# Performance work log

Measured on AMD Instinct MI355X. Metric: run time of the kernel, lower is better.

The kernel has to match this reference:

```python
import jax, jax.numpy as jnp
import numpy as np

D = 1024
B, S = 4, 4096


def setup_inputs() -> dict:
    key = jax.random.key(0)
    ks = jax.random.split(key, 5)
    scale = 1.0 / np.sqrt(D)  # ~ torch Linear init magnitude
    return {
        "x": jax.random.normal(ks[0], (B, S, D), dtype=jnp.float32),
        "Wa": jax.random.normal(ks[1], (D, D), dtype=jnp.float32) * scale,
        "Wb": jax.random.normal(ks[2], (D, D), dtype=jnp.float32) * scale,
        "Wc": jax.random.normal(ks[3], (D, D), dtype=jnp.float32) * scale,
        "Wd": jax.random.normal(ks[4], (D, D), dtype=jnp.float32) * scale,
    }


def reference(x, Wa, Wb, Wc, Wd):
    # torch nn.Linear(bias=False): y = x @ W.T, W is [out, in]
    A = jax.nn.relu(jnp.einsum("bsd,ed->bse", x, Wa))
    Bm = jax.nn.relu(jnp.einsum("bsd,ed->bse", x, Wb))
    C = jax.nn.relu(jnp.einsum("bsd,ed->bse", x, Wc))
    cmp_matrix = jnp.einsum("bse,bte->bst", A, Bm)  # [B,S,S] unnormalized scores
    out = jnp.einsum("bst,bte->bse", cmp_matrix, C)
    return jax.nn.relu(jnp.einsum("bsd,ed->bse", out, Wd))
```

## Files before the change

### kernel.cpp

```cpp
#include <hip/hip_runtime.h>
#include <hip/hip_bf16.h>

#define D_ 1024
#define B_ 4
#define S_ 4096

typedef __attribute__((ext_vector_type(8))) short bf16x8;
typedef __attribute__((ext_vector_type(4))) float f32x4;
typedef __attribute__((ext_vector_type(4))) unsigned int u32x4;
typedef __attribute__((ext_vector_type(4))) unsigned short u16x4;

__device__ __forceinline__ unsigned short f2bf(float f) {
    unsigned int u = __builtin_bit_cast(unsigned int, f);
    u = u + 0x7fffu + ((u >> 16) & 1u);
    return (unsigned short)(u >> 16);
}
__device__ __forceinline__ unsigned int pk2(float a, float b) {
    return (unsigned int)f2bf(a) | ((unsigned int)f2bf(b) << 16);
}
__device__ __forceinline__ float bf2f(unsigned short h) {
    unsigned int u = ((unsigned int)h) << 16;
    return __builtin_bit_cast(float, u);
}
__device__ __forceinline__ void gload16(const void* g, void* l) {
    __builtin_amdgcn_global_load_lds(
        (const __attribute__((address_space(1))) void*)g,
        (__attribute__((address_space(3))) void*)l, 16, 0, 0);
}

__device__ __forceinline__ void conv8(const float* s, unsigned short* d, size_t j) {
    f32x4 v0 = *(const f32x4*)(s + j);
    f32x4 v1 = *(const f32x4*)(s + j + 4);
    u32x4 o;
    o[0] = pk2(v0[0], v0[1]);
    o[1] = pk2(v0[2], v0[3]);
    o[2] = pk2(v1[0], v1[1]);
    o[3] = pk2(v1[2], v1[3]);
    *(u32x4*)(d + j) = o;
}

__global__ __launch_bounds__(256)
void conv_all(const float* __restrict__ x, const float* __restrict__ Wb,
              const float* __restrict__ Wc,
              unsigned short* __restrict__ xb, unsigned short* __restrict__ wbb,
              unsigned short* __restrict__ wcb, int n8x, int n8w) {
    int i = blockIdx.x * blockDim.x + threadIdx.x;
    const int stride = gridDim.x * blockDim.x;
    const int ntot = n8x + 2 * n8w;
    for (; i < ntot; i += stride) {
        if (i < n8x)                conv8(x,  xb,  (size_t)i * 8);
        else if (i < n8x + n8w)     conv8(Wb, wbb, (size_t)(i - n8x) * 8);
        else                        conv8(Wc, wcb, (size_t)(i - n8x - n8w) * 8);
    }
}

__global__ __launch_bounds__(256)
void reduce_convw(const unsigned short* __restrict__ P, unsigned short* __restrict__ E,
                  const float* __restrict__ Wd, const float* __restrict__ Wa,
                  unsigned short* __restrict__ wdb, unsigned short* __restrict__ wab,
                  int n8e, int n8w) {
    int t = blockIdx.x * blockDim.x + threadIdx.x;
    const int stride = gridDim.x * blockDim.x;
    const int DD = D_ * D_;
    const int ntot = n8e + 2 * n8w;
    for (; t < ntot; t += stride) {
        if (t < n8e) {
            size_t idx = (size_t)t * 8;
            int b = (int)(idx / DD);
            size_t i = idx % DD;
            float s[8];
#pragma unroll
            for (int k = 0; k < 8; ++k) s[k] = 0.f;
#pragma unroll
            for (int seg = 0; seg < 4; ++seg) {
                const unsigned short* p = P + (size_t)(b * 4 + seg) * DD + i;
                u16x4 v0 = *(const u16x4*)p;
                u16x4 v1 = *(const u16x4*)(p + 4);
#pragma unroll
                for (int k = 0; k < 4; ++k) { s[k] += bf2f(v0[k]); s[4 + k] += bf2f(v1[k]); }
            }
            u16x4 o0, o1;
#pragma unroll
            for (int k = 0; k < 4; ++k) { o0[k] = f2bf(s[k]); o1[k] = f2bf(s[4 + k]); }
            *(u16x4*)(E + idx) = o0;
            *(u16x4*)(E + idx + 4) = o1;
        } else if (t < n8e + n8w) {
            conv8(Wd, wdb, (size_t)(t - n8e) * 8);
        } else {
            conv8(Wa, wab, (size_t)(t - n8e - n8w) * 8);
        }
    }
}

#define BM 128
#define BN 128
#define BK 64
#define NTHR 256

template<bool OUT_F32, bool TRANS, bool RELU>
__global__ __launch_bounds__(NTHR)
void gemm_nt(const unsigned short* __restrict__ Ap, const unsigned short* __restrict__ Bp,
             void* __restrict__ Op, int M, int N, int K, int klen, int split,
             long long sA, long long sB, long long sO)
{
    __shared__ char lds_a[BM * BK * 2];
    __shared__ char lds_b[BN * BK * 2];

    const int tid   = threadIdx.x;
    const int bz    = blockIdx.z;
    const int batch = bz / split;
    const int k0    = (bz % split) * klen;
    const int bm    = blockIdx.y * BM;
    const int bn    = blockIdx.x * BN;

    const unsigned short* Abase = Ap + (size_t)batch * sA + (size_t)bm * K;
    const unsigned short* Bbase = Bp + (size_t)batch * sB + (size_t)bn * K;

    const int lane = tid & 63;
    const int wave = tid >> 6;
    const int wm   = (wave >> 1) * 64;
    const int wn   = (wave & 1) * 64;
    const int l16  = lane & 15;
    const int lhi  = lane >> 4;

    const int schnk = (lane & 7) ^ (lane >> 3);
    const char* gA0 = (const char*)(Abase + (size_t)(wave * 32 + (lane >> 3)) * K) + schnk * 16;
    const char* gB0 = (const char*)(Bbase + (size_t)(wave * 32 + (lane >> 3)) * K) + schnk * 16;
    char* lA0 = lds_a + wave * 4096;
    char* lB0 = lds_b + wave * 4096;

    f32x4 acc[4][4];
#pragma unroll
    for (int i = 0; i < 4; ++i)
#pragma unroll
        for (int j = 0; j < 4; ++j)
            acc[i][j] = (f32x4){0.f, 0.f, 0.f, 0.f};

    for (int kt = k0; kt < k0 + klen; kt += BK) {
#pragma unroll
        for (int p = 0; p < 4; ++p)
            gload16(gA0 + ((size_t)p * 8 * K + kt) * 2, lA0 + p * 1024);
#pragma unroll
        for (int p = 0; p < 4; ++p)
            gload16(gB0 + ((size_t)p * 8 * K + kt) * 2, lB0 + p * 1024);
        __syncthreads();
#pragma unroll
        for (int kk = 0; kk < BK / 32; ++kk) {
            bf16x8 af[4], bfr[4];
#pragma unroll
            for (int i = 0; i < 4; ++i) {
                int row = wm + i * 16 + l16;
                int byt = (row * 128 + kk * 64 + lhi * 16) ^ ((row & 7) << 4);
                af[i] = *(const bf16x8*)(lds_a + byt);
            }
#pragma unroll
            for (int j = 0; j < 4; ++j) {
                int row = wn + j * 16 + l16;
                int byt = (row * 128 + kk * 64 + lhi * 16) ^ ((row & 7) << 4);
                bfr[j] = *(const bf16x8*)(lds_b + byt);
            }
#pragma unroll
            for (int i = 0; i < 4; ++i)
#pragma unroll
                for (int j = 0; j < 4; ++j)
                    acc[i][j] = __builtin_amdgcn_mfma_f32_16x16x32_bf16(af[i], bfr[j], acc[i][j], 0, 0, 0);
        }
        __syncthreads();
    }

    const size_t obase = (size_t)bz * (size_t)sO;
    if constexpr (!TRANS) {
#pragma unroll
        for (int i = 0; i < 4; ++i) {
            const int m0 = bm + wm + i * 16 + lhi * 4;
#pragma unroll
            for (int j = 0; j < 4; ++j) {
                const int n = bn + wn + j * 16 + l16;
#pragma unroll
                for (int r = 0; r < 4; ++r) {
                    float v = acc[i][j][r];
                    if constexpr (RELU) v = fmaxf(v, 0.f);
                    size_t addr = obase + (size_t)(m0 + r) * N + n;
                    if constexpr (OUT_F32) ((float*)Op)[addr] = v;
                    else ((unsigned short*)Op)[addr] = f2bf(v);
                }
            }
        }
    } else {
#pragma unroll
        for (int i = 0; i < 4; ++i) {
            const int m0 = bm + wm + i * 16 + lhi * 4;
#pragma unroll
            for (int j = 0; j < 4; ++j) {
                const int n = bn + wn + j * 16 + l16;
                u16x4 h;
#pragma unroll
                for (int r = 0; r < 4; ++r) {
                    float v = acc[i][j][r];
                    if constexpr (RELU) v = fmaxf(v, 0.f);
                    h[r] = f2bf(v);
                }
                *(u16x4*)((unsigned short*)Op + obase + (size_t)n * M + m0) = h;
            }
        }
    }
}

#define CTILE 65536
#define CBOFF 32768

template<bool OUT_F32, bool TRANS, bool RELU>
__global__ __launch_bounds__(512, 2)
void gemm256(const unsigned short* __restrict__ Ap, const unsigned short* __restrict__ Bp,
             void* __restrict__ Op, int M, int N, int K, int klen, int split,
             long long sA, long long sB, long long sO)
{
    __shared__ char lds[131072];
    const int tid  = threadIdx.x;
    const int wave = tid >> 6;
    const int lane = tid & 63;

    const int gx = gridDim.x, gy = gridDim.y;
    const int f   = blockIdx.x + gx * (blockIdx.y + gy * blockIdx.z);
    const int nwg = gx * gy * (int)gridDim.z;
    const int s   = (f & 7) * (nwg >> 3) + (f >> 3);
    const int lx  = s % gx;
    const int lyz = s / gx;
    const int ly  = lyz % gy;
    const int lz  = lyz / gy;

    const int batch = lz / split;
    const int k0    = (lz % split) * klen;
    const int bm    = ly * 256;
    const int bn    = lx * 256;

    const int wm  = (wave >> 2) * 128;
    const int wn  = (wave & 3) * 64;
    const int l16 = lane & 15, lhi = lane >> 4;

    const unsigned short* Abase = Ap + (size_t)batch * sA + (size_t)bm * K;
    const unsigned short* Bbase = Bp + (size_t)batch * sB + (size_t)bn * K;
    const int srow  = lane >> 3;
    const int schnk = (lane & 7) ^ srow;
    const size_t K2 = (size_t)K * 2;
    const char* gA = (const char*)Abase + (size_t)srow * K2 + (size_t)schnk * 16 + (size_t)k0 * 2;
    const char* gB = (const char*)Bbase + (size_t)srow * K2 + (size_t)schnk * 16 + (size_t)k0 * 2;

    const int lxor = (l16 & 7) << 4;
    const int aX = (wm + l16) * 128 + lhi * 16;
    const int bX = (wn + l16) * 128 + lhi * 16;
    const char* aB00 = lds + 0 * CTILE + ((aX + 0 * 64) ^ lxor);
    const char* aB01 = lds + 0 * CTILE + ((aX + 1 * 64) ^ lxor);
    const char* aB10 = lds + 1 * CTILE + ((aX + 0 * 64) ^ lxor);
    const char* aB11 = lds + 1 * CTILE + ((aX + 1 * 64) ^ lxor);
    const char* bB00 = lds + 0 * CTILE + CBOFF + ((bX + 0 * 64) ^ lxor);
    const char* bB01 = lds + 0 * CTILE + CBOFF + ((bX + 1 * 64) ^ lxor);
    const char* bB10 = lds + 1 * CTILE + CBOFF + ((bX + 0 * 64) ^ lxor);
    const char* bB11 = lds + 1 * CTILE + CBOFF + ((bX + 1 * 64) ^ lxor);

    f32x4 acc[8][4];
#pragma unroll
    for (int i = 0; i < 8; ++i)
#pragma unroll
        for (int j = 0; j < 4; ++j)
            acc[i][j] = (f32x4){0.f, 0.f, 0.f, 0.f};

    bf16x8 a[4][2], b0[2][2], b1[2][2];

    auto stageA2 = [&](int c, int t, int h) {
#pragma unroll
        for (int p = 0; p < 2; ++p)
            gload16(gA + (size_t)t * 128 + (size_t)(h * 128 + wave * 16 + p * 8) * K2,
                    lds + c * CTILE + h * 16384 + wave * 2048 + p * 1024);
    };
    auto stageB2 = [&](int c, int t, int h) {
#pragma unroll
        for (int p = 0; p < 2; ++p)
            gload16(gB + (size_t)t * 128 + (size_t)(h * 128 + wave * 16 + p * 8) * K2,
                    lds + c * CTILE + CBOFF + h * 16384 + wave * 2048 + p * 1024);
    };
    auto ldAh = [&](int c, int mh, int lo) {
        const char* base0 = c ? aB10 : aB00;
        const char* base1 = c ? aB11 : aB01;
#pragma unroll
        for (int i4 = 0; i4 < 2; ++i4) {
            const int imm = (mh * 64 + (lo + i4) * 16) * 128;
            a[lo + i4][0] = *(const bf16x8*)(base0 + imm);
            a[lo + i4][1] = *(const bf16x8*)(base1 + imm);
        }
    };
    auto ldBh = [&](int c, int nh, bf16x8 (&bb)[2][2], int j2) {
        const char* base0 = c ? bB10 : bB00;
        const char* base1 = c ? bB11 : bB01;
        const int imm = (nh * 32 + j2 * 16) * 128;
        bb[j2][0] = *(const bf16x8*)(base0 + imm);
        bb[j2][1] = *(const bf16x8*)(base1 + imm);
    };
    auto ldB = [&](int c, int nh, bf16x8 (&bb)[2][2]) {
        ldBh(c, nh, bb, 0); ldBh(c, nh, bb, 1);
    };
    auto mmH = [&](int mh, int nh, bf16x8 (&bb)[2][2], int lo) {
        __builtin_amdgcn_s_setprio(1);
#pragma unroll
        for (int i4 = 0; i4 < 2; ++i4)
#pragma unroll
            for (int j2 = 0; j2 < 2; ++j2)
#pragma unroll
                for (int kk = 0; kk < 2; ++kk)
                    acc[mh * 4 + lo + i4][nh * 2 + j2] = __builtin_amdgcn_mfma_f32_16x16x32_bf16(
                        a[lo + i4][kk], bb[j2][kk], acc[mh * 4 + lo + i4][nh * 2 + j2], 0, 0, 0);
        __builtin_amdgcn_s_setprio(0);
    };
    auto mm = [&](int mh, int nh, bf16x8 (&bb)[2][2]) { mmH(mh, nh, bb, 0); mmH(mh, nh, bb, 2); };

#define BAR()   __builtin_amdgcn_s_barrier()
#define LGKM0() asm volatile("s_waitcnt lgkmcnt(0)" ::: "memory")
#define VM2()   asm volatile("s_waitcnt vmcnt(2)" ::: "memory")
#define VM4()   asm volatile("s_waitcnt vmcnt(4)" ::: "memory")
#define VM6()   asm volatile("s_waitcnt vmcnt(6)" ::: "memory")

    const int NT = klen / 64;
    stageB2(0, 0, 0); stageB2(0, 0, 1); stageA2(0, 0, 0); stageA2(0, 0, 1);
    stageB2(1, 1, 0); stageB2(1, 1, 1); stageA2(1, 1, 0);
    VM6();
    BAR();
    ldB(0, 0, b0); ldAh(0, 0, 0); ldAh(0, 0, 2);

    for (int itr = 0; itr < NT / 2; ++itr) {
        const int t1  = 2 * itr + 1;
        const int tp0 = (2 * itr + 2) % NT;
        const int tp1 = (2 * itr + 3) % NT;
        LGKM0(); mmH(0, 0, b0, 0);
        ldBh(0, 1, b1, 0);
        mmH(0, 0, b0, 2);
        ldBh(0, 1, b1, 1); stageA2(1, t1, 1);
        BAR();
        LGKM0(); mmH(0, 1, b1, 0);
        ldAh(0, 1, 0);
        mmH(0, 1, b1, 2);
        ldAh(0, 1, 2); VM4();
        BAR();
        LGKM0(); mm(1, 0, b0);
        ldB(1, 0, b0); stageB2(0, tp0, 0); VM2();
        BAR();
        LGKM0(); mmH(1, 1, b1, 0);
        ldAh(1, 0, 0);
        mmH(1, 1, b1, 2);
        ldAh(1, 0, 2); stageB2(0, tp0, 1); stageA2(0, tp0, 0);
        BAR();
        LGKM0(); mmH(0, 0, b0, 0);
        ldBh(1, 1, b1, 0);
        mmH(0, 0, b0, 2);
        ldBh(1, 1, b1, 1); stageA2(0, tp0, 1);
        BAR();
        LGKM0(); mmH(0, 1, b1, 0);
        ldAh(1, 1, 0);
        mmH(0, 1, b1, 2);
        ldAh(1, 1, 2); VM4();
        BAR();
        LGKM0(); mm(1, 0, b0);
        ldB(0, 0, b0); stageB2(1, tp1, 0); VM2();
        BAR();
        LGKM0(); mmH(1, 1, b1, 0);
        ldAh(0, 0, 0);
        mmH(1, 1, b1, 2);
        ldAh(0, 0, 2); stageB2(1, tp1, 1); stageA2(1, tp1, 0);
        BAR();
    }
    asm volatile("s_waitcnt vmcnt(0)" ::: "memory");

    const size_t obase = (size_t)lz * (size_t)sO;
    if constexpr (!TRANS) {
#pragma unroll
        for (int i = 0; i < 8; ++i) {
            const int m0 = bm + wm + i * 16 + lhi * 4;
#pragma unroll
            for (int j = 0; j < 4; ++j) {
                const int n = bn + wn + j * 16 + l16;
#pragma unroll
                for (int r = 0; r < 4; ++r) {
                    float v = acc[i][j][r];
                    if constexpr (RELU) v = fmaxf(v, 0.f);
                    size_t addr = obase + (size_t)(m0 + r) * N + n;
                    if constexpr (OUT_F32) ((float*)Op)[addr] = v;
                    else ((unsigned short*)Op)[addr] = f2bf(v);
                }
            }
        }
    } else {
#pragma unroll
        for (int i = 0; i < 8; ++i) {
            const int m0 = bm + wm + i * 16 + lhi * 4;
#pragma unroll
            for (int j = 0; j < 4; ++j) {
                const int n = bn + wn + j * 16 + l16;
                u16x4 h;
#pragma unroll
                for (int r = 0; r < 4; ++r) {
                    float v = acc[i][j][r];
                    if constexpr (RELU) v = fmaxf(v, 0.f);
                    h[r] = f2bf(v);
                }
                *(u16x4*)((unsigned short*)Op + obase + (size_t)n * M + m0) = h;
            }
        }
    }
#undef BAR
#undef LGKM0
#undef VM2
#undef VM4
#undef VM6
}

extern "C" void kernel_launch(void* const* d_in, const int* in_sizes, int n_in,
                              void* d_out, int out_size, void* d_ws, size_t ws_size,
                              hipStream_t stream) {
    (void)in_sizes; (void)n_in; (void)out_size; (void)ws_size;
    const float* x  = (const float*)d_in[0];
    const float* Wa = (const float*)d_in[1];
    const float* Wb = (const float*)d_in[2];
    const float* Wc = (const float*)d_in[3];
    const float* Wd = (const float*)d_in[4];

    const long long SD  = (long long)S_ * D_;
    const long long DD2 = (long long)D_ * D_;
    const size_t MB = 1024 * 1024;

    unsigned short* BC    = (unsigned short*)d_ws;
    unsigned short* Enorm = (unsigned short*)d_ws;
    unsigned short* Ao    = (unsigned short*)d_ws;
    unsigned short* Ft    = (unsigned short*)((char*)d_ws + 32 * MB);
    unsigned short* Wdb   = (unsigned short*)((char*)d_ws + 40 * MB);
    unsigned short* Wab   = (unsigned short*)((char*)d_ws + 42 * MB);
    char* ob = (char*)d_out;
    unsigned short* xb  = (unsigned short*)ob;
    unsigned short* Pp  = (unsigned short*)(ob + 32 * MB);
    unsigned short* Wbb = (unsigned short*)(ob + 56 * MB);
    unsigned short* Wcb = (unsigned short*)(ob + 58 * MB);

    dim3 blk256(256, 1, 1);
    dim3 blk512(512, 1, 1);
    dim3 gBC(2048 / 256, S_ / 256, B_);
    dim3 gE(D_ / 256, D_ / 256, B_ * 4);
    dim3 gS(D_ / 256, S_ / 256, B_);
    dim3 gF(D_ / BN, D_ / BM, B_);

    const int n8x = (B_ * S_ * D_) / 8;
    const int n8w = (D_ * D_) / 8;
    const int n8e = (B_ * D_ * D_) / 8;

    conv_all<<<2048, blk256, 0, stream>>>(x, Wb, Wc, xb, Wbb, Wcb, n8x, n8w);
    gemm256<false, true,  true ><<<gBC, blk512, 0, stream>>>(xb, Wbb, BC, S_, 2048, D_, D_, 1, SD, 0, 2 * SD);
    gemm256<false, false, false><<<gE, blk512, 0, stream>>>(BC, BC + SD, Pp, D_, D_, S_, S_ / 4, 4, 2 * SD, 2 * SD, DD2);
    reduce_convw<<<1024, blk256, 0, stream>>>(Pp, Enorm, Wd, Wa, Wdb, Wab, n8e, n8w);
    gemm_nt<false, true,  false><<<gF, blk256, 0, stream>>>(Enorm, Wdb, Ft, D_, D_, D_, D_, 1, DD2, 0, DD2);
    gemm256<false, false, true ><<<gS, blk512, 0, stream>>>(xb, Wab, Ao, S_, D_, D_, D_, 1, SD, 0, SD);
    gemm256<true,  false, true ><<<gS, blk512, 0, stream>>>(Ao, Ft, (float*)d_out, S_, D_, D_, D_, 1, SD, DD2, SD);
}
```

Measured before the change: 237.7 us.

## Add 16-wave 256x256 GEMM variant and use it for the BC and E stages

Introduces a 1024-thread (16-wave) version of the 256x256-tile bf16 MFMA GEMM, where each wave computes a 64x64 sub-tile, with a reworked double-buffered LDS staging and barrier schedule. The two large GEMMs (B/C projection and the split-K A^T-style product) now launch this kernel instead of the 512-thread version. The aim is more waves in flight to hide LDS and global latency and to spread MFMA work. The cost is more barriers per k-step, a smaller per-wave tile with less register reuse, and tighter register limits from 1024-thread launch bounds.

```diff
diff --git a/kernel.cpp b/kernel.cpp
--- a/kernel.cpp
+++ b/kernel.cpp
@@ -412,6 +412,200 @@
 #undef VM6
 }
 
+template<bool OUT_F32, bool TRANS, bool RELU>
+__global__ __launch_bounds__(1024, 4)
+void gemm256w16(const unsigned short* __restrict__ Ap, const unsigned short* __restrict__ Bp,
+                void* __restrict__ Op, int M, int N, int K, int klen, int split,
+                long long sA, long long sB, long long sO)
+{
+    __shared__ char lds[131072];
+    const int tid  = threadIdx.x;
+    const int wave = tid >> 6;
+    const int lane = tid & 63;
+
+    const int gx = gridDim.x, gy = gridDim.y;
+    const int f   = blockIdx.x + gx * (blockIdx.y + gy * blockIdx.z);
+    const int nwg = gx * gy * (int)gridDim.z;
+    const int s   = (f & 7) * (nwg >> 3) + (f >> 3);
+    const int lx  = s % gx;
+    const int lyz = s / gx;
+    const int ly  = lyz % gy;
+    const int lz  = lyz / gy;
+
+    const int batch = lz / split;
+    const int k0    = (lz % split) * klen;
+    const int bm    = ly * 256;
+    const int bn    = lx * 256;
+
+    const int wm  = (wave >> 2) * 64;
+    const int wn  = (wave & 3) * 64;
+    const int l16 = lane & 15, lhi = lane >> 4;
+
+    const unsigned short* Abase = Ap + (size_t)batch * sA + (size_t)bm * K;
+    const unsigned short* Bbase = Bp + (size_t)batch * sB + (size_t)bn * K;
+    const int srowB = tid >> 3;
+    const int schnk = (lane & 7) ^ (lane >> 3);
+    const size_t K2 = (size_t)K * 2;
+    const char* gA = (const char*)Abase + (size_t)srowB * K2 + (size_t)schnk * 16 + (size_t)k0 * 2;
+    const char* gB = (const char*)Bbase + (size_t)srowB * K2 + (size_t)schnk * 16 + (size_t)k0 * 2;
+
+    const int lxor = (l16 & 7) << 4;
+    const int aX = (wm + l16) * 128 + lhi * 16;
+    const int bX = (wn + l16) * 128 + lhi * 16;
+    const char* aB00 = lds + 0 * CTILE + ((aX + 0 * 64) ^ lxor);
+    const char* aB01 = lds + 0 * CTILE + ((aX + 1 * 64) ^ lxor);
+    const char* aB10 = lds + 1 * CTILE + ((aX + 0 * 64) ^ lxor);
+    const char* aB11 = lds + 1 * CTILE + ((aX + 1 * 64) ^ lxor);
+    const char* bB00 = lds + 0 * CTILE + CBOFF + ((bX + 0 * 64) ^ lxor);
+    const char* bB01 = lds + 0 * CTILE + CBOFF + ((bX + 1 * 64) ^ lxor);
+    const char* bB10 = lds + 1 * CTILE + CBOFF + ((bX + 0 * 64) ^ lxor);
+    const char* bB11 = lds + 1 * CTILE + CBOFF + ((bX + 1 * 64) ^ lxor);
+
+    f32x4 acc[4][4];
+#pragma unroll
+    for (int i = 0; i < 4; ++i)
+#pragma unroll
+        for (int j = 0; j < 4; ++j)
+            acc[i][j] = (f32x4){0.f, 0.f, 0.f, 0.f};
+
+    bf16x8 a[2][2], b0[2][2], b1[2][2];
+
+    auto stageA2 = [&](int c, int t, int h) {
+        gload16(gA + (size_t)t * 128 + (size_t)(h * 128) * K2,
+                lds + c * CTILE + h * 16384 + wave * 1024);
+    };
+    auto stageB2 = [&](int c, int t, int h) {
+        gload16(gB + (size_t)t * 128 + (size_t)(h * 128) * K2,
+                lds + c * CTILE + CBOFF + h * 16384 + wave * 1024);
+    };
+    auto ldAh = [&](int c, int mh, int q) {
+        const char* base0 = c ? aB10 : aB00;
+        const char* base1 = c ? aB11 : aB01;
+        const int imm = (mh * 32 + q * 16) * 128;
+        a[q][0] = *(const bf16x8*)(base0 + imm);
+        a[q][1] = *(const bf16x8*)(base1 + imm);
+    };
+    auto ldBh = [&](int c, int nh, bf16x8 (&bb)[2][2], int j2) {
+        const char* base0 = c ? bB10 : bB00;
+        const char* base1 = c ? bB11 : bB01;
+        const int imm = (nh * 32 + j2 * 16) * 128;
+        bb[j2][0] = *(const bf16x8*)(base0 + imm);
+        bb[j2][1] = *(const bf16x8*)(base1 + imm);
+    };
+    auto ldB = [&](int c, int nh, bf16x8 (&bb)[2][2]) {
+        ldBh(c, nh, bb, 0); ldBh(c, nh, bb, 1);
+    };
+    auto mmH = [&](int mh, int nh, bf16x8 (&bb)[2][2], int q) {
+        __builtin_amdgcn_s_setprio(1);
+#pragma unroll
+        for (int j2 = 0; j2 < 2; ++j2)
+#pragma unroll
+            for (int kk = 0; kk < 2; ++kk)
+                acc[mh * 2 + q][nh * 2 + j2] = __builtin_amdgcn_mfma_f32_16x16x32_bf16(
+                    a[q][kk], bb[j2][kk], acc[mh * 2 + q][nh * 2 + j2], 0, 0, 0);
+        __builtin_amdgcn_s_setprio(0);
+    };
+    auto mm = [&](int mh, int nh, bf16x8 (&bb)[2][2]) { mmH(mh, nh, bb, 0); mmH(mh, nh, bb, 1); };
+
+#define BAR()   __builtin_amdgcn_s_barrier()
+#define LGKM0() asm volatile("s_waitcnt lgkmcnt(0)" ::: "memory")
+#define VM1()   asm volatile("s_waitcnt vmcnt(1)" ::: "memory")
+#define VM2()   asm volatile("s_waitcnt vmcnt(2)" ::: "memory")
+#define VM3()   asm volatile("s_waitcnt vmcnt(3)" ::: "memory")
+
+    const int NT = klen / 64;
+    stageB2(0, 0, 0); stageB2(0, 0, 1); stageA2(0, 0, 0); stageA2(0, 0, 1);
+    stageB2(1, 1, 0); stageB2(1, 1, 1); stageA2(1, 1, 0);
+    VM3();
+    BAR();
+    ldB(0, 0, b0); ldAh(0, 0, 0); ldAh(0, 0, 1);
+
+    for (int itr = 0; itr < NT / 2; ++itr) {
+        const int t1  = 2 * itr + 1;
+        const int tp0 = (2 * itr + 2) % NT;
+        const int tp1 = (2 * itr + 3) % NT;
+        LGKM0(); mmH(0, 0, b0, 0);
+        ldBh(0, 1, b1, 0);
+        mmH(0, 0, b0, 1);
+        ldBh(0, 1, b1, 1); stageA2(1, t1, 1);
+        BAR();
+        LGKM0(); mmH(0, 1, b1, 0);
+        ldAh(0, 1, 0);
+        mmH(0, 1, b1, 1);
+        ldAh(0, 1, 1); VM2();
+        BAR();
+        LGKM0(); mm(1, 0, b0);
+        ldB(1, 0, b0); stageB2(0, tp0, 0); VM1();
+        BAR();
+        LGKM0(); mmH(1, 1, b1, 0);
+        ldAh(1, 0, 0);
+        mmH(1, 1, b1, 1);
+        ldAh(1, 0, 1); stageB2(0, tp0, 1); stageA2(0, tp0, 0);
+        BAR();
+        LGKM0(); mmH(0, 0, b0, 0);
+        ldBh(1, 1, b1, 0);
+        mmH(0, 0, b0, 1);
+        ldBh(1, 1, b1, 1); stageA2(0, tp0, 1);
+        BAR();
+        LGKM0(); mmH(0, 1, b1, 0);
+        ldAh(1, 1, 0);
+        mmH(0, 1, b1, 1);
+        ldAh(1, 1, 1); VM2();
+        BAR();
+        LGKM0(); mm(1, 0, b0);
+        ldB(0, 0, b0); stageB2(1, tp1, 0); VM1();
+        BAR();
+        LGKM0(); mmH(1, 1, b1, 0);
+        ldAh(0, 0, 0);
+        mmH(1, 1, b1, 1);
+        ldAh(0, 0, 1); stageB2(1, tp1, 1); stageA2(1, tp1, 0);
+        BAR();
+    }
+    asm volatile("s_waitcnt vmcnt(0)" ::: "memory");
+
+    const size_t obase = (size_t)lz * (size_t)sO;
+    if constexpr (!TRANS) {
+#pragma unroll
+        for (int i = 0; i < 4; ++i) {
+            const int m0 = bm + wm + i * 16 + lhi * 4;
+#pragma unroll
+            for (int j = 0; j < 4; ++j) {
+                const int n = bn + wn + j * 16 + l16;
+#pragma unroll
+                for (int r = 0; r < 4; ++r) {
+                    float v = acc[i][j][r];
+                    if constexpr (RELU) v = fmaxf(v, 0.f);
+                    size_t addr = obase + (size_t)(m0 + r) * N + n;
+                    if constexpr (OUT_F32) ((float*)Op)[addr] = v;
+                    else ((unsigned short*)Op)[addr] = f2bf(v);
+                }
+            }
+        }
+    } else {
+#pragma unroll
+        for (int i = 0; i < 4; ++i) {
+            const int m0 = bm + wm + i * 16 + lhi * 4;
+#pragma unroll
+            for (int j = 0; j < 4; ++j) {
+                const int n = bn + wn + j * 16 + l16;
+                u16x4 h;
+#pragma unroll
+                for (int r = 0; r < 4; ++r) {
+                    float v = acc[i][j][r];
+                    if constexpr (RELU) v = fmaxf(v, 0.f);
+                    h[r] = f2bf(v);
+                }
+                *(u16x4*)((unsigned short*)Op + obase + (size_t)n * M + m0) = h;
+            }
+        }
+    }
+#undef BAR
+#undef LGKM0
+#undef VM1
+#undef VM2
+#undef VM3
+}
+
 extern "C" void kernel_launch(void* const* d_in, const int* in_sizes, int n_in,
                               void* d_out, int out_size, void* d_ws, size_t ws_size,
                               hipStream_t stream) {
@@ -440,6 +634,7 @@
 
     dim3 blk256(256, 1, 1);
     dim3 blk512(512, 1, 1);
+    dim3 blk1024(1024, 1, 1);
     dim3 gBC(2048 / 256, S_ / 256, B_);
     dim3 gE(D_ / 256, D_ / 256, B_ * 4);
     dim3 gS(D_ / 256, S_ / 256, B_);
@@ -450,8 +645,8 @@
     const int n8e = (B_ * D_ * D_) / 8;
 
     conv_all<<<2048, blk256, 0, stream>>>(x, Wb, Wc, xb, Wbb, Wcb, n8x, n8w);
-    gemm256<false, true,  true ><<<gBC, blk512, 0, stream>>>(xb, Wbb, BC, S_, 2048, D_, D_, 1, SD, 0, 2 * SD);
-    gemm256<false, false, false><<<gE, blk512, 0, stream>>>(BC, BC + SD, Pp, D_, D_, S_, S_ / 4, 4, 2 * SD, 2 * SD, DD2);
+    gemm256w16<false, true,  true ><<<gBC, blk1024, 0, stream>>>(xb, Wbb, BC, S_, 2048, D_, D_, 1, SD, 0, 2 * SD);
+    gemm256w16<false, false, false><<<gE, blk1024, 0, stream>>>(BC, BC + SD, Pp, D_, D_, S_, S_ / 4, 4, 2 * SD, 2 * SD, DD2);
     reduce_convw<<<1024, blk256, 0, stream>>>(Pp, Enorm, Wd, Wa, Wdb, Wab, n8e, n8w);
     gemm_nt<false, true,  false><<<gF, blk256, 0, stream>>>(Enorm, Wdb, Ft, D_, D_, D_, D_, 1, DD2, 0, DD2);
     gemm256<false, false, true ><<<gS, blk512, 0, stream>>>(xb, Wab, Ao, S_, D_, D_, D_, 1, SD, 0, SD);
```

Measured after the change: 241.3 us. About the same (+1.5%).
